# Performance work log

Hardware: AMD Instinct MI355X
Metric: run time of the kernel (lower is better)

Reference implementation:

```python
import jax, jax.numpy as jnp
import numpy as np

N_FEAT = 256
NUM_HEADS = 8
EPS = 1e-12  # torch F.normalize default eps


def setup_inputs() -> dict:
    key = jax.random.key(0)
    k1, k2, k3 = jax.random.split(key, 3)
    b, c, h, w = 1, N_FEAT, 64, 64
    x = jax.random.normal(k1, (b, c, h, w), dtype=jnp.float32)
    # 1x1 convs == channel GEMMs; store as (out_ch, in_ch) matrices
    w_qkv = jax.random.normal(k2, (3 * c, c), dtype=jnp.float32) * (1.0 / np.sqrt(c))
    w_proj = jax.random.normal(k3, (c, c), dtype=jnp.float32) * (1.0 / np.sqrt(c))
    temperature = jnp.ones((NUM_HEADS, 1, 1), dtype=jnp.float32)
    return {"x": x, "w_qkv": w_qkv, "w_proj": w_proj, "temperature": temperature}


def _l2norm(t):
    n = jnp.linalg.norm(t, axis=-1, keepdims=True)
    return t / jnp.maximum(n, EPS)


def reference(x, w_qkv, w_proj, temperature):
    b, c, h, w = x.shape
    heads = temperature.shape[0]
    d = c // heads
    hw = h * w
    xf = x.reshape(b, c, hw)
    # qkv 1x1 conv: (b, 3c, hw)
    qkv = jnp.einsum('oc,bcs->bos', w_qkv, xf)
    qkv = qkv.reshape(b, 3, heads, d, hw)
    q, k, v = qkv[:, 0], qkv[:, 1], qkv[:, 2]  # (b, heads, d, hw)
    q = jnp.swapaxes(q, -2, -1)  # (b, heads, hw, d)
    k = jnp.swapaxes(k, -2, -1)
    v = jnp.swapaxes(v, -2, -1)
    q = _l2norm(q)
    k = _l2norm(k)
    attn = jnp.einsum('bhsd,bhtd->bhst', q, k) * temperature[None]  # (b, heads, hw, hw)
    attn = jax.nn.softmax(attn, axis=-1)
    out = jnp.einsum('bhst,bhtd->bhsd', attn, v)  # (b, heads, hw, d)
    # faithful to torch: permute(0,2,1,3).reshape(b,c,h,w)
    out = out.transpose(0, 2, 1, 3).reshape(b, c, h, w)
    out = jnp.einsum('oc,bchw->bohw', w_proj, out)
    return out
```

## Files before the change

kernel.cpp:

```cpp
#include <hip/hip_runtime.h>
#include <stdint.h>

#define HW 4096
#define NH 8
#define NSPLIT 4
#define TSPLIT (HW / NSPLIT)

typedef __attribute__((ext_vector_type(8))) short short8;
typedef __attribute__((ext_vector_type(4))) short s4b;
typedef __attribute__((ext_vector_type(4))) float floatx4;

__device__ inline float bf2f(uint16_t u) {
  union { uint32_t i; float f; } v; v.i = ((uint32_t)u) << 16; return v.f;
}
__device__ inline float bflo(uint32_t u) {
  union { uint32_t i; float f; } v; v.i = u << 16; return v.f;
}
__device__ inline float bfhi(uint32_t u) {
  union { uint32_t i; float f; } v; v.i = u & 0xFFFF0000u; return v.f;
}
__device__ inline uint16_t f2bf(float f) {
  union { float f; uint32_t i; } v; v.f = f;
  uint32_t u = v.i; u += 0x7fffu + ((u >> 16) & 1u); return (uint16_t)(u >> 16);
}
__device__ inline uint32_t pk2(float a, float b) {
  return (uint32_t)f2bf(a) | ((uint32_t)f2bf(b) << 16);
}
__device__ inline uint32_t asu(float f) { union { float f; uint32_t i; } v; v.f = f; return v.i; }
__device__ inline uint32_t pk2r(float a, float b) {
#if __has_builtin(__builtin_amdgcn_cvt_pk_bf16_f32)
  union { short2 s; uint32_t u; } x;
  x.s = __builtin_amdgcn_cvt_pk_bf16_f32(a, b);
  return x.u;
#else
  return __builtin_amdgcn_perm(asu(b) + 0x8000u, asu(a) + 0x8000u, 0x07060302u);
#endif
}
__device__ inline s4b mk_s4(uint32_t lo, uint32_t hi) {
  union { uint32_t u[2]; s4b s; } x; x.u[0] = lo; x.u[1] = hi; return x.s;
}
__device__ inline floatx4 mfma16(s4b a, s4b b, floatx4 c) {
#if __has_builtin(__builtin_amdgcn_mfma_f32_16x16x16bf16_1k)
  return __builtin_amdgcn_mfma_f32_16x16x16bf16_1k(a, b, c, 0, 0, 0);
#else
  floatx4 d = c;
  asm volatile("v_mfma_f32_16x16x16_bf16 %0, %1, %2, %0" : "+v"(d) : "v"(a), "v"(b));
  return d;
#endif
}
__device__ inline bool is_f32(const uint32_t* Tp32) { return (Tp32[0] & 0xFFFFu) == 0u; }
__device__ inline float read_temp(const void* Tp, int h) {
  if (is_f32((const uint32_t*)Tp)) return ((const float*)Tp)[h];
  return bf2f(((const uint16_t*)Tp)[h]);
}

__global__ __launch_bounds__(256) void k_transpose(const void* __restrict__ X,
                                                   uint16_t* __restrict__ Xt,
                                                   const uint32_t* __restrict__ Tp32) {
  __shared__ uint16_t tile[64 * 66];
  int t = threadIdx.x;
  int s0 = blockIdx.x * 64, c0 = blockIdx.y * 64;
  {
    int cl = t >> 2, sc = (t & 3) * 16;
    uint32_t* l32 = (uint32_t*)tile;
    int base = (cl * 66 + sc) >> 1;
    if (is_f32(Tp32)) {
      const float4* x4 = (const float4*)((const float*)X + (c0 + cl) * HW + s0 + sc);
      float4 a = x4[0], b = x4[1], c = x4[2], d = x4[3];
      l32[base + 0] = pk2(a.x, a.y); l32[base + 1] = pk2(a.z, a.w);
      l32[base + 2] = pk2(b.x, b.y); l32[base + 3] = pk2(b.z, b.w);
      l32[base + 4] = pk2(c.x, c.y); l32[base + 5] = pk2(c.z, c.w);
      l32[base + 6] = pk2(d.x, d.y); l32[base + 7] = pk2(d.z, d.w);
    } else {
      const uint4* xp = (const uint4*)((const uint16_t*)X + (c0 + cl) * HW + s0 + sc);
      uint4 a = xp[0], b = xp[1];
      l32[base + 0] = a.x; l32[base + 1] = a.y; l32[base + 2] = a.z; l32[base + 3] = a.w;
      l32[base + 4] = b.x; l32[base + 5] = b.y; l32[base + 6] = b.z; l32[base + 7] = b.w;
    }
  }
  __syncthreads();
  {
    int sl = t >> 2, cc = (t & 3) * 16;
    uint32_t wbuf[8];
#pragma unroll
    for (int j = 0; j < 8; ++j) {
      uint32_t lo = tile[(cc + 2 * j) * 66 + sl];
      uint32_t hi = tile[(cc + 2 * j + 1) * 66 + sl];
      wbuf[j] = lo | (hi << 16);
    }
    uint4* op = (uint4*)(Xt + (s0 + sl) * 256 + c0 + cc);
    op[0] = make_uint4(wbuf[0], wbuf[1], wbuf[2], wbuf[3]);
    op[1] = make_uint4(wbuf[4], wbuf[5], wbuf[6], wbuf[7]);
  }
}

__global__ __launch_bounds__(256) void k_gemm_qkv(const void* __restrict__ A,
                                                  const uint16_t* __restrict__ Bt,
                                                  const void* __restrict__ Tp,
                                                  uint16_t* __restrict__ Qr,
                                                  uint16_t* __restrict__ Kr,
                                                  uint16_t* __restrict__ Vr) {
  __shared__ uint16_t sA[128 * 64];
  __shared__ uint16_t sB[64 * 64];
  int tid = threadIdx.x;
  int w = tid >> 6, lane = tid & 63, lm = lane & 15, qd = lane >> 4;
  int n0 = blockIdx.x * 64, m0 = blockIdx.y * 128;
  bool aF32 = is_f32((const uint32_t*)Tp);
  floatx4 acc[2][4];
#pragma unroll
  for (int i = 0; i < 2; ++i)
#pragma unroll
    for (int j = 0; j < 4; ++j) acc[i][j] = (floatx4){0.f, 0.f, 0.f, 0.f};

  for (int k0 = 0; k0 < 256; k0 += 64) {
    __syncthreads();
#pragma unroll
    for (int r = 0; r < 4; ++r) {
      int ch = r * 256 + tid; int row = ch >> 3, c8 = ch & 7;
      uint4 v;
      if (aF32) {
        const float4* s4 = (const float4*)((const float*)A + (m0 + row) * 256 + k0 + c8 * 8);
        float4 a = s4[0], b = s4[1];
        v = make_uint4(pk2(a.x, a.y), pk2(a.z, a.w), pk2(b.x, b.y), pk2(b.z, b.w));
      } else {
        v = *(const uint4*)((const uint16_t*)A + (m0 + row) * 256 + k0 + c8 * 8);
      }
      *(uint4*)(&sA[row * 64 + (c8 ^ (row & 7)) * 8]) = v;
    }
#pragma unroll
    for (int r = 0; r < 2; ++r) {
      int ch = r * 256 + tid; int row = ch >> 3, c8 = ch & 7;
      uint4 v = *(const uint4*)(Bt + (n0 + row) * 256 + k0 + c8 * 8);
      *(uint4*)(&sB[row * 64 + (c8 ^ (row & 7)) * 8]) = v;
    }
    __syncthreads();
#pragma unroll
    for (int kk = 0; kk < 2; ++kk) {
      short8 af[2];
#pragma unroll
      for (int mt = 0; mt < 2; ++mt) {
        int row = w * 32 + mt * 16 + lm;
        af[mt] = *(const short8*)(&sA[row * 64 + ((kk * 4 + qd) ^ (row & 7)) * 8]);
      }
#pragma unroll
      for (int nt = 0; nt < 4; ++nt) {
        int row = nt * 16 + lm;
        short8 bf = *(const short8*)(&sB[row * 64 + ((kk * 4 + qd) ^ (row & 7)) * 8]);
#pragma unroll
        for (int mt = 0; mt < 2; ++mt)
          acc[mt][nt] = __builtin_amdgcn_mfma_f32_16x16x32_bf16(af[mt], bf, acc[mt][nt], 0, 0, 0);
      }
    }
  }
  int ow = m0 + w * 32;
  int type = ow >> 8;
  int hh = (ow >> 5) & 7;
  float tv = read_temp(Tp, hh);
#pragma unroll
  for (int nt = 0; nt < 4; ++nt) {
    int s = n0 + nt * 16 + lm;
    if (type < 2) {
      float ssq = 0.f;
#pragma unroll
      for (int mt = 0; mt < 2; ++mt)
#pragma unroll
        for (int r = 0; r < 4; ++r) ssq += acc[mt][nt][r] * acc[mt][nt][r];
      ssq += __shfl_xor(ssq, 16, 64);
      ssq += __shfl_xor(ssq, 32, 64);
      float sc = (type == 0 ? tv : 1.0f) / fmaxf(sqrtf(ssq), 1e-12f);
      uint16_t* dst = (type == 0 ? Qr : Kr) + ((hh << 12) + s) * 32;
#pragma unroll
      for (int mt = 0; mt < 2; ++mt)
        *(uint2*)(dst + mt * 16 + qd * 4) =
            make_uint2(pk2r(acc[mt][nt][0] * sc, acc[mt][nt][1] * sc),
                       pk2r(acc[mt][nt][2] * sc, acc[mt][nt][3] * sc));
    } else {
#pragma unroll
      for (int mt = 0; mt < 2; ++mt)
#pragma unroll
        for (int r = 0; r < 4; ++r)
          Vr[(hh * 32 + mt * 16 + qd * 4 + r) * HW + s] = f2bf(acc[mt][nt][r]);
    }
  }
}

__global__ __launch_bounds__(256, 4) void k_attn(const uint16_t* __restrict__ Qr,
                                                 const uint16_t* __restrict__ Kr,
                                                 const uint16_t* __restrict__ Vr,
                                                 const void* __restrict__ Tp,
                                                 uint16_t* __restrict__ Op,
                                                 float* __restrict__ Lp) {
  __shared__ uint16_t sK[128 * 32];
  __shared__ uint16_t sV[32 * 128];
  int tid = threadIdx.x;
  int w = tid >> 6, lane = tid & 63, lm = lane & 15, qd = lane >> 4;
  int bid = blockIdx.x;
  int h = bid & 7;
  int j = bid >> 3;
  int sp = j & 3;
  int qb = j >> 2;
  int srow = qb * 128 + w * 32;
  const float c1 = 1.44269504088896340736f;
  float c2 = fabsf(read_temp(Tp, h)) * c1;
  short8 qf0 = *(const short8*)(Qr + ((h << 12) + srow + lm) * 32 + qd * 8);
  short8 qf1 = *(const short8*)(Qr + ((h << 12) + srow + 16 + lm) * 32 + qd * 8);
  const uint16_t* Kg = Kr + (h << 12) * 32;
  const uint16_t* Vg = Vr + (h * 32) * HW;
  floatx4 o00 = {0.f, 0.f, 0.f, 0.f}, o01 = {0.f, 0.f, 0.f, 0.f};
  floatx4 o10 = {0.f, 0.f, 0.f, 0.f}, o11 = {0.f, 0.f, 0.f, 0.f};
  floatx4 l0 = {0.f, 0.f, 0.f, 0.f}, l1 = {0.f, 0.f, 0.f, 0.f};
  const s4b ones = mk_s4(0x3F803F80u, 0x3F803F80u);

  int rK = tid >> 2, cK = tid & 3;
  uint16_t* dK0 = &sK[rK * 32 + (cK ^ ((rK >> 1) & 3)) * 8];
  uint16_t* dK1 = &sK[(rK + 64) * 32 + (cK ^ (((rK + 64) >> 1) & 3)) * 8];
  const uint16_t* gK0 = Kg + (sp * TSPLIT + rK) * 32 + cK * 8;
  const uint16_t* gK1 = gK0 + 64 * 32;
  int dV = tid >> 4, cV = tid & 15;
  bool sw = dV & 1;
  uint16_t* dV0 = &sV[dV * 128 + (cV ^ ((dV >> 1) & 7)) * 8];
  uint16_t* dV1 = &sV[(dV + 16) * 128 + (cV ^ (((dV + 16) >> 1) & 7)) * 8];
  const uint16_t* gV0 = Vg + dV * HW + sp * TSPLIT + cV * 8;
  const uint16_t* gV1 = gV0 + 16 * HW;

  uint4 rk0 = *(const uint4*)gK0, rk1 = *(const uint4*)gK1;
  uint4 rv0 = *(const uint4*)gV0, rv1 = *(const uint4*)gV1;

  for (int i = 0; i < TSPLIT / 128; ++i) {
    __syncthreads();
    *(uint4*)dK0 = rk0;
    *(uint4*)dK1 = rk1;
    *(uint4*)dV0 = sw ? make_uint4(rv0.z, rv0.w, rv0.x, rv0.y) : rv0;
    *(uint4*)dV1 = sw ? make_uint4(rv1.z, rv1.w, rv1.x, rv1.y) : rv1;
    if (i + 1 < TSPLIT / 128) {
      gK0 += 128 * 32; gK1 += 128 * 32; gV0 += 128; gV1 += 128;
      rk0 = *(const uint4*)gK0; rk1 = *(const uint4*)gK1;
      rv0 = *(const uint4*)gV0; rv1 = *(const uint4*)gV1;
    }
    asm volatile("s_waitcnt lgkmcnt(0)\n\ts_barrier" ::: "memory");
#pragma unroll
    for (int nt = 0; nt < 8; ++nt) {
      int krow = nt * 16 + lm;
      short8 kf = *(const short8*)(&sK[krow * 32 + (qd ^ ((lm >> 1) & 3)) * 8]);
      int gp = (nt * 4 + qd) ^ lm;
      s4b v0 = *(const s4b*)(&sV[lm * 128 + gp * 4]);
      s4b v1 = *(const s4b*)(&sV[(lm + 16) * 128 + gp * 4]);
      floatx4 z = {0.f, 0.f, 0.f, 0.f};
      floatx4 sv = __builtin_amdgcn_mfma_f32_16x16x32_bf16(kf, qf0, z, 0, 0, 0);
      float p0 = __builtin_amdgcn_exp2f(fmaf(sv[0], c1, -c2));
      float p1 = __builtin_amdgcn_exp2f(fmaf(sv[1], c1, -c2));
      float p2 = __builtin_amdgcn_exp2f(fmaf(sv[2], c1, -c2));
      float p3 = __builtin_amdgcn_exp2f(fmaf(sv[3], c1, -c2));
      s4b pa = mk_s4(pk2r(p0, p1), pk2r(p2, p3));
      o00 = mfma16(pa, v0, o00);
      o01 = mfma16(pa, v1, o01);
      l0 = mfma16(pa, ones, l0);
      sv = __builtin_amdgcn_mfma_f32_16x16x32_bf16(kf, qf1, z, 0, 0, 0);
      p0 = __builtin_amdgcn_exp2f(fmaf(sv[0], c1, -c2));
      p1 = __builtin_amdgcn_exp2f(fmaf(sv[1], c1, -c2));
      p2 = __builtin_amdgcn_exp2f(fmaf(sv[2], c1, -c2));
      p3 = __builtin_amdgcn_exp2f(fmaf(sv[3], c1, -c2));
      pa = mk_s4(pk2r(p0, p1), pk2r(p2, p3));
      o10 = mfma16(pa, v0, o10);
      o11 = mfma16(pa, v1, o11);
      l1 = mfma16(pa, ones, l1);
    }
  }
  int sb = (sp * NH + h) * HW + srow;
  uint16_t* op = Op + (size_t)sb * 32;
#pragma unroll
  for (int r = 0; r < 4; ++r) {
    op[(qd * 4 + r) * 32 + lm] = f2bf(o00[r]);
    op[(qd * 4 + r) * 32 + 16 + lm] = f2bf(o01[r]);
    op[(16 + qd * 4 + r) * 32 + lm] = f2bf(o10[r]);
    op[(16 + qd * 4 + r) * 32 + 16 + lm] = f2bf(o11[r]);
  }
  if (lm == 0) {
#pragma unroll
    for (int r = 0; r < 4; ++r) {
      Lp[sb + qd * 4 + r] = l0[r];
      Lp[sb + 16 + qd * 4 + r] = l1[r];
    }
  }
}

__global__ __launch_bounds__(256) void k_comb(const uint16_t* __restrict__ Op,
                                              const float* __restrict__ Lp,
                                              uint16_t* __restrict__ Yt) {
  int gid = blockIdx.x * 256 + threadIdx.x;
  int g = gid >> 1, d0 = (gid & 1) * 16;
  int h = g >> 12, s = g & 4095;
  float L = 0.f;
  float a[16];
#pragma unroll
  for (int j = 0; j < 16; ++j) a[j] = 0.f;
#pragma unroll
  for (int sp = 0; sp < NSPLIT; ++sp) {
    int gj = sp * NH * HW + g;
    L += Lp[gj];
    const uint4* p = (const uint4*)(Op + (size_t)gj * 32 + d0);
    uint4 x = p[0], y = p[1];
    a[0] += bflo(x.x); a[1] += bfhi(x.x); a[2] += bflo(x.y); a[3] += bfhi(x.y);
    a[4] += bflo(x.z); a[5] += bfhi(x.z); a[6] += bflo(x.w); a[7] += bfhi(x.w);
    a[8] += bflo(y.x); a[9] += bfhi(y.x); a[10] += bflo(y.y); a[11] += bfhi(y.y);
    a[12] += bflo(y.z); a[13] += bfhi(y.z); a[14] += bflo(y.w); a[15] += bfhi(y.w);
  }
  float inv = __builtin_amdgcn_rcpf(L);
  int pbase = ((s & 15) << 8) + h * 32 + d0;
  int cp = s >> 4;
#pragma unroll
  for (int j = 0; j < 16; ++j) Yt[(pbase + j) * 256 + cp] = f2bf(a[j] * inv);
}

__global__ __launch_bounds__(256) void k_gemm_proj(const void* __restrict__ A,
                                                   const uint16_t* __restrict__ Bt,
                                                   void* __restrict__ C,
                                                   const uint32_t* __restrict__ Tp32) {
  __shared__ uint16_t sA[64 * 64];
  __shared__ uint16_t sB[64 * 64];
  int tid = threadIdx.x;
  int w = tid >> 6, lane = tid & 63, lm = lane & 15, qd = lane >> 4;
  int n0 = blockIdx.x * 64, m0 = blockIdx.y * 64;
  bool aF32 = is_f32(Tp32);
  floatx4 acc[4];
#pragma unroll
  for (int i = 0; i < 4; ++i) acc[i] = (floatx4){0.f, 0.f, 0.f, 0.f};

  for (int k0 = 0; k0 < 256; k0 += 64) {
    __syncthreads();
#pragma unroll
    for (int r = 0; r < 2; ++r) {
      int ch = r * 256 + tid; int row = ch >> 3, c8 = ch & 7;
      uint4 v;
      if (aF32) {
        const float4* s4 = (const float4*)((const float*)A + (m0 + row) * 256 + k0 + c8 * 8);
        float4 a = s4[0], b = s4[1];
        v = make_uint4(pk2(a.x, a.y), pk2(a.z, a.w), pk2(b.x, b.y), pk2(b.z, b.w));
      } else {
        v = *(const uint4*)((const uint16_t*)A + (m0 + row) * 256 + k0 + c8 * 8);
      }
      *(uint4*)(&sA[row * 64 + (c8 ^ (row & 7)) * 8]) = v;
    }
#pragma unroll
    for (int r = 0; r < 2; ++r) {
      int ch = r * 256 + tid; int row = ch >> 3, c8 = ch & 7;
      uint4 v = *(const uint4*)(Bt + (n0 + row) * 256 + k0 + c8 * 8);
      *(uint4*)(&sB[row * 64 + (c8 ^ (row & 7)) * 8]) = v;
    }
    __syncthreads();
#pragma unroll
    for (int kk = 0; kk < 2; ++kk) {
      int arow = w * 16 + lm;
      short8 af = *(const short8*)(&sA[arow * 64 + ((kk * 4 + qd) ^ (arow & 7)) * 8]);
#pragma unroll
      for (int nt = 0; nt < 4; ++nt) {
        int row = nt * 16 + lm;
        short8 bf = *(const short8*)(&sB[row * 64 + ((kk * 4 + qd) ^ (row & 7)) * 8]);
        acc[nt] = __builtin_amdgcn_mfma_f32_16x16x32_bf16(af, bf, acc[nt], 0, 0, 0);
      }
    }
  }
  bool f32o = is_f32(Tp32);
#pragma unroll
  for (int nt = 0; nt < 4; ++nt)
#pragma unroll
    for (int r = 0; r < 4; ++r) {
      int row = m0 + w * 16 + qd * 4 + r;
      int col = n0 + nt * 16 + lm;
      if (f32o) ((float*)C)[row * HW + col] = acc[nt][r];
      else ((uint16_t*)C)[row * HW + col] = f2bf(acc[nt][r]);
    }
}

extern "C" void kernel_launch(void* const* d_in, const int* in_sizes, int n_in,
                              void* d_out, int out_size, void* d_ws, size_t ws_size,
                              hipStream_t stream) {
  const void* X  = d_in[0];
  const void* Wq = d_in[1];
  const void* Wp = d_in[2];
  const void* Tp = d_in[3];
  const uint32_t* Tp32 = (const uint32_t*)Tp;
  uint16_t* ws = (uint16_t*)d_ws;
  uint16_t* Xt = ws;
  uint16_t* Qr = Xt + 4096 * 256;
  uint16_t* Kr = Qr + NH * HW * 32;
  uint16_t* Vr = Kr + NH * HW * 32;
  uint16_t* Yt = Vr + NH * 32 * HW;
  uint16_t* Op = Yt + 4096 * 256;
  float* Lp = (float*)(Op + (size_t)NSPLIT * NH * HW * 32);

  k_transpose<<<dim3(64, 4), 256, 0, stream>>>(X, Xt, Tp32);
  k_gemm_qkv<<<dim3(64, 6), 256, 0, stream>>>(Wq, Xt, Tp, Qr, Kr, Vr);
  k_attn<<<dim3(1024), 256, 0, stream>>>(Qr, Kr, Vr, Tp, Op, Lp);
  k_comb<<<dim3(256), 256, 0, stream>>>(Op, Lp, Yt);
  k_gemm_proj<<<dim3(64, 4), 256, 0, stream>>>(Wp, Yt, d_out, Tp32);
}
```

Measured before the change: 122.2 us.

## Fuse input transpose into QKV GEMM, enlarge attention KV tile, halve proj tile

Removes the standalone transpose kernel: the QKV GEMM now loads raw channel-major X, transposes it through a padded shared tile and writes the swizzled B operand directly. This drops one launch and a global round trip of the transposed X, at the cost of an extra barrier and shared-memory pass in every k-step, repeated across the six M-blocks. The attention kernel stages 256 keys/values per iteration instead of 128, halving barrier count but doubling LDS use, which may reduce occupancy. The projection GEMM uses 32-wide N tiles to launch twice as many blocks.

```diff
diff --git a/kernel.cpp b/kernel.cpp
--- a/kernel.cpp
+++ b/kernel.cpp
@@ -54,54 +54,15 @@
   return bf2f(((const uint16_t*)Tp)[h]);
 }
 
-__global__ __launch_bounds__(256) void k_transpose(const void* __restrict__ X,
-                                                   uint16_t* __restrict__ Xt,
-                                                   const uint32_t* __restrict__ Tp32) {
-  __shared__ uint16_t tile[64 * 66];
-  int t = threadIdx.x;
-  int s0 = blockIdx.x * 64, c0 = blockIdx.y * 64;
-  {
-    int cl = t >> 2, sc = (t & 3) * 16;
-    uint32_t* l32 = (uint32_t*)tile;
-    int base = (cl * 66 + sc) >> 1;
-    if (is_f32(Tp32)) {
-      const float4* x4 = (const float4*)((const float*)X + (c0 + cl) * HW + s0 + sc);
-      float4 a = x4[0], b = x4[1], c = x4[2], d = x4[3];
-      l32[base + 0] = pk2(a.x, a.y); l32[base + 1] = pk2(a.z, a.w);
-      l32[base + 2] = pk2(b.x, b.y); l32[base + 3] = pk2(b.z, b.w);
-      l32[base + 4] = pk2(c.x, c.y); l32[base + 5] = pk2(c.z, c.w);
-      l32[base + 6] = pk2(d.x, d.y); l32[base + 7] = pk2(d.z, d.w);
-    } else {
-      const uint4* xp = (const uint4*)((const uint16_t*)X + (c0 + cl) * HW + s0 + sc);
-      uint4 a = xp[0], b = xp[1];
-      l32[base + 0] = a.x; l32[base + 1] = a.y; l32[base + 2] = a.z; l32[base + 3] = a.w;
-      l32[base + 4] = b.x; l32[base + 5] = b.y; l32[base + 6] = b.z; l32[base + 7] = b.w;
-    }
-  }
-  __syncthreads();
-  {
-    int sl = t >> 2, cc = (t & 3) * 16;
-    uint32_t wbuf[8];
-#pragma unroll
-    for (int j = 0; j < 8; ++j) {
-      uint32_t lo = tile[(cc + 2 * j) * 66 + sl];
-      uint32_t hi = tile[(cc + 2 * j + 1) * 66 + sl];
-      wbuf[j] = lo | (hi << 16);
-    }
-    uint4* op = (uint4*)(Xt + (s0 + sl) * 256 + c0 + cc);
-    op[0] = make_uint4(wbuf[0], wbuf[1], wbuf[2], wbuf[3]);
-    op[1] = make_uint4(wbuf[4], wbuf[5], wbuf[6], wbuf[7]);
-  }
-}
-
-__global__ __launch_bounds__(256) void k_gemm_qkv(const void* __restrict__ A,
-                                                  const uint16_t* __restrict__ Bt,
+__global__ __launch_bounds__(256) void k_gemm_qkv(const void* __restrict__ X,
+                                                  const void* __restrict__ A,
                                                   const void* __restrict__ Tp,
                                                   uint16_t* __restrict__ Qr,
                                                   uint16_t* __restrict__ Kr,
                                                   uint16_t* __restrict__ Vr) {
   __shared__ uint16_t sA[128 * 64];
   __shared__ uint16_t sB[64 * 64];
+  __shared__ uint16_t sXr[64 * 66];
   int tid = threadIdx.x;
   int w = tid >> 6, lane = tid & 63, lm = lane & 15, qd = lane >> 4;
   int n0 = blockIdx.x * 64, m0 = blockIdx.y * 128;
@@ -114,6 +75,24 @@
 
   for (int k0 = 0; k0 < 256; k0 += 64) {
     __syncthreads();
+    {
+      int cl = tid >> 2, sc = (tid & 3) * 16;
+      uint32_t* l32 = (uint32_t*)sXr;
+      int base = (cl * 66 + sc) >> 1;
+      if (aF32) {
+        const float4* x4 = (const float4*)((const float*)X + (k0 + cl) * HW + n0 + sc);
+        float4 a = x4[0], b = x4[1], c = x4[2], d = x4[3];
+        l32[base + 0] = pk2(a.x, a.y); l32[base + 1] = pk2(a.z, a.w);
+        l32[base + 2] = pk2(b.x, b.y); l32[base + 3] = pk2(b.z, b.w);
+        l32[base + 4] = pk2(c.x, c.y); l32[base + 5] = pk2(c.z, c.w);
+        l32[base + 6] = pk2(d.x, d.y); l32[base + 7] = pk2(d.z, d.w);
+      } else {
+        const uint4* xp = (const uint4*)((const uint16_t*)X + (k0 + cl) * HW + n0 + sc);
+        uint4 a = xp[0], b = xp[1];
+        l32[base + 0] = a.x; l32[base + 1] = a.y; l32[base + 2] = a.z; l32[base + 3] = a.w;
+        l32[base + 4] = b.x; l32[base + 5] = b.y; l32[base + 6] = b.z; l32[base + 7] = b.w;
+      }
+    }
 #pragma unroll
     for (int r = 0; r < 4; ++r) {
       int ch = r * 256 + tid; int row = ch >> 3, c8 = ch & 7;
@@ -127,11 +106,21 @@
       }
       *(uint4*)(&sA[row * 64 + (c8 ^ (row & 7)) * 8]) = v;
     }
-#pragma unroll
-    for (int r = 0; r < 2; ++r) {
-      int ch = r * 256 + tid; int row = ch >> 3, c8 = ch & 7;
-      uint4 v = *(const uint4*)(Bt + (n0 + row) * 256 + k0 + c8 * 8);
-      *(uint4*)(&sB[row * 64 + (c8 ^ (row & 7)) * 8]) = v;
+    __syncthreads();
+    {
+      int sl = tid >> 2, cs = (tid & 3) * 16;
+      uint32_t wb[8];
+#pragma unroll
+      for (int j = 0; j < 8; ++j) {
+        uint32_t lo = sXr[(cs + 2 * j) * 66 + sl];
+        uint32_t hi = sXr[(cs + 2 * j + 1) * 66 + sl];
+        wb[j] = lo | (hi << 16);
+      }
+      int c8 = cs >> 3;
+      *(uint4*)(&sB[sl * 64 + ((c8 ^ (sl & 7))) * 8]) =
+          make_uint4(wb[0], wb[1], wb[2], wb[3]);
+      *(uint4*)(&sB[sl * 64 + (((c8 + 1) ^ (sl & 7))) * 8]) =
+          make_uint4(wb[4], wb[5], wb[6], wb[7]);
     }
     __syncthreads();
 #pragma unroll
@@ -190,8 +179,8 @@
                                                  const void* __restrict__ Tp,
                                                  uint16_t* __restrict__ Op,
                                                  float* __restrict__ Lp) {
-  __shared__ uint16_t sK[128 * 32];
-  __shared__ uint16_t sV[32 * 128];
+  __shared__ uint16_t sK[256 * 32];
+  __shared__ uint16_t sV[32 * 256];
   int tid = threadIdx.x;
   int w = tid >> 6, lane = tid & 63, lm = lane & 15, qd = lane >> 4;
   int bid = blockIdx.x;
@@ -212,39 +201,51 @@
   const s4b ones = mk_s4(0x3F803F80u, 0x3F803F80u);
 
   int rK = tid >> 2, cK = tid & 3;
-  uint16_t* dK0 = &sK[rK * 32 + (cK ^ ((rK >> 1) & 3)) * 8];
-  uint16_t* dK1 = &sK[(rK + 64) * 32 + (cK ^ (((rK + 64) >> 1) & 3)) * 8];
-  const uint16_t* gK0 = Kg + (sp * TSPLIT + rK) * 32 + cK * 8;
-  const uint16_t* gK1 = gK0 + 64 * 32;
-  int dV = tid >> 4, cV = tid & 15;
-  bool sw = dV & 1;
-  uint16_t* dV0 = &sV[dV * 128 + (cV ^ ((dV >> 1) & 7)) * 8];
-  uint16_t* dV1 = &sV[(dV + 16) * 128 + (cV ^ (((dV + 16) >> 1) & 7)) * 8];
-  const uint16_t* gV0 = Vg + dV * HW + sp * TSPLIT + cV * 8;
-  const uint16_t* gV1 = gV0 + 16 * HW;
-
-  uint4 rk0 = *(const uint4*)gK0, rk1 = *(const uint4*)gK1;
-  uint4 rv0 = *(const uint4*)gV0, rv1 = *(const uint4*)gV1;
-
-  for (int i = 0; i < TSPLIT / 128; ++i) {
-    __syncthreads();
-    *(uint4*)dK0 = rk0;
-    *(uint4*)dK1 = rk1;
-    *(uint4*)dV0 = sw ? make_uint4(rv0.z, rv0.w, rv0.x, rv0.y) : rv0;
-    *(uint4*)dV1 = sw ? make_uint4(rv1.z, rv1.w, rv1.x, rv1.y) : rv1;
-    if (i + 1 < TSPLIT / 128) {
-      gK0 += 128 * 32; gK1 += 128 * 32; gV0 += 128; gV1 += 128;
-      rk0 = *(const uint4*)gK0; rk1 = *(const uint4*)gK1;
-      rv0 = *(const uint4*)gV0; rv1 = *(const uint4*)gV1;
+  uint16_t* dK[4];
+  const uint16_t* gK[4];
+#pragma unroll
+  for (int r = 0; r < 4; ++r) {
+    int row = rK + 64 * r;
+    dK[r] = &sK[row * 32 + (cK ^ ((row >> 1) & 3)) * 8];
+    gK[r] = Kg + (sp * TSPLIT + row) * 32 + cK * 8;
+  }
+  int dVb = tid >> 5, cVx = tid & 31;
+  bool sw = dVb & 1;
+  uint16_t* dVp[4];
+  const uint16_t* gVp[4];
+#pragma unroll
+  for (int r = 0; r < 4; ++r) {
+    int d = dVb + 8 * r;
+    dVp[r] = &sV[d * 256 + (cVx ^ ((d >> 1) & 7)) * 8];
+    gVp[r] = Vg + d * HW + sp * TSPLIT + cVx * 8;
+  }
+  uint4 rk[4], rv[4];
+#pragma unroll
+  for (int r = 0; r < 4; ++r) { rk[r] = *(const uint4*)gK[r]; rv[r] = *(const uint4*)gVp[r]; }
+
+  for (int i = 0; i < TSPLIT / 256; ++i) {
+    __syncthreads();
+#pragma unroll
+    for (int r = 0; r < 4; ++r) *(uint4*)dK[r] = rk[r];
+#pragma unroll
+    for (int r = 0; r < 4; ++r)
+      *(uint4*)dVp[r] = sw ? make_uint4(rv[r].z, rv[r].w, rv[r].x, rv[r].y) : rv[r];
+    if (i + 1 < TSPLIT / 256) {
+#pragma unroll
+      for (int r = 0; r < 4; ++r) {
+        gK[r] += 256 * 32; gVp[r] += 256;
+        rk[r] = *(const uint4*)gK[r];
+        rv[r] = *(const uint4*)gVp[r];
+      }
     }
     asm volatile("s_waitcnt lgkmcnt(0)\n\ts_barrier" ::: "memory");
 #pragma unroll
-    for (int nt = 0; nt < 8; ++nt) {
+    for (int nt = 0; nt < 16; ++nt) {
       int krow = nt * 16 + lm;
       short8 kf = *(const short8*)(&sK[krow * 32 + (qd ^ ((lm >> 1) & 3)) * 8]);
       int gp = (nt * 4 + qd) ^ lm;
-      s4b v0 = *(const s4b*)(&sV[lm * 128 + gp * 4]);
-      s4b v1 = *(const s4b*)(&sV[(lm + 16) * 128 + gp * 4]);
+      s4b v0 = *(const s4b*)(&sV[lm * 256 + gp * 4]);
+      s4b v1 = *(const s4b*)(&sV[(lm + 16) * 256 + gp * 4]);
       floatx4 z = {0.f, 0.f, 0.f, 0.f};
       floatx4 sv = __builtin_amdgcn_mfma_f32_16x16x32_bf16(kf, qf0, z, 0, 0, 0);
       float p0 = __builtin_amdgcn_exp2f(fmaf(sv[0], c1, -c2));
@@ -317,14 +318,14 @@
                                                    void* __restrict__ C,
                                                    const uint32_t* __restrict__ Tp32) {
   __shared__ uint16_t sA[64 * 64];
-  __shared__ uint16_t sB[64 * 64];
+  __shared__ uint16_t sB[32 * 64];
   int tid = threadIdx.x;
   int w = tid >> 6, lane = tid & 63, lm = lane & 15, qd = lane >> 4;
-  int n0 = blockIdx.x * 64, m0 = blockIdx.y * 64;
+  int n0 = blockIdx.x * 32, m0 = blockIdx.y * 64;
   bool aF32 = is_f32(Tp32);
-  floatx4 acc[4];
-#pragma unroll
-  for (int i = 0; i < 4; ++i) acc[i] = (floatx4){0.f, 0.f, 0.f, 0.f};
+  floatx4 acc[2];
+  acc[0] = (floatx4){0.f, 0.f, 0.f, 0.f};
+  acc[1] = (floatx4){0.f, 0.f, 0.f, 0.f};
 
   for (int k0 = 0; k0 < 256; k0 += 64) {
     __syncthreads();
@@ -341,9 +342,8 @@
       }
       *(uint4*)(&sA[row * 64 + (c8 ^ (row & 7)) * 8]) = v;
     }
-#pragma unroll
-    for (int r = 0; r < 2; ++r) {
-      int ch = r * 256 + tid; int row = ch >> 3, c8 = ch & 7;
+    {
+      int row = tid >> 3, c8 = tid & 7;
       uint4 v = *(const uint4*)(Bt + (n0 + row) * 256 + k0 + c8 * 8);
       *(uint4*)(&sB[row * 64 + (c8 ^ (row & 7)) * 8]) = v;
     }
@@ -353,7 +353,7 @@
       int arow = w * 16 + lm;
       short8 af = *(const short8*)(&sA[arow * 64 + ((kk * 4 + qd) ^ (arow & 7)) * 8]);
 #pragma unroll
-      for (int nt = 0; nt < 4; ++nt) {
+      for (int nt = 0; nt < 2; ++nt) {
         int row = nt * 16 + lm;
         short8 bf = *(const short8*)(&sB[row * 64 + ((kk * 4 + qd) ^ (row & 7)) * 8]);
         acc[nt] = __builtin_amdgcn_mfma_f32_16x16x32_bf16(af, bf, acc[nt], 0, 0, 0);
@@ -362,7 +362,7 @@
   }
   bool f32o = is_f32(Tp32);
 #pragma unroll
-  for (int nt = 0; nt < 4; ++nt)
+  for (int nt = 0; nt < 2; ++nt)
 #pragma unroll
     for (int r = 0; r < 4; ++r) {
       int row = m0 + w * 16 + qd * 4 + r;
@@ -381,17 +381,15 @@
   const void* Tp = d_in[3];
   const uint32_t* Tp32 = (const uint32_t*)Tp;
   uint16_t* ws = (uint16_t*)d_ws;
-  uint16_t* Xt = ws;
-  uint16_t* Qr = Xt + 4096 * 256;
+  uint16_t* Qr = ws;
   uint16_t* Kr = Qr + NH * HW * 32;
   uint16_t* Vr = Kr + NH * HW * 32;
   uint16_t* Yt = Vr + NH * 32 * HW;
   uint16_t* Op = Yt + 4096 * 256;
   float* Lp = (float*)(Op + (size_t)NSPLIT * NH * HW * 32);
 
-  k_transpose<<<dim3(64, 4), 256, 0, stream>>>(X, Xt, Tp32);
-  k_gemm_qkv<<<dim3(64, 6), 256, 0, stream>>>(Wq, Xt, Tp, Qr, Kr, Vr);
+  k_gemm_qkv<<<dim3(64, 6), 256, 0, stream>>>(X, Wq, Tp, Qr, Kr, Vr);
   k_attn<<<dim3(1024), 256, 0, stream>>>(Qr, Kr, Vr, Tp, Op, Lp);
   k_comb<<<dim3(256), 256, 0, stream>>>(Op, Lp, Yt);
-  k_gemm_proj<<<dim3(64, 4), 256, 0, stream>>>(Wp, Yt, d_out, Tp32);
-}
+  k_gemm_proj<<<dim3(128, 4), 256, 0, stream>>>(Wp, Yt, d_out, Tp32);
+}
```

After: 126.3 us. 1.03x slower.
